# Kernel optimization log

Hardware: AMD Instinct MI355X
Metric: run time of the kernel (lower is better)

Reference implementation:

```python
import jax, jax.numpy as jnp
import numpy as np

LN_EPS = 1e-5   # torch nn.LayerNorm default
R_EPS = 1e-8    # eps used in log(R.clamp(min=eps))


def layernorm(x, g, b):
    mu = jnp.mean(x, axis=-1, keepdims=True)
    var = jnp.var(x, axis=-1, keepdims=True)
    return (x - mu) * jax.lax.rsqrt(var + LN_EPS) * g + b


def setup_inputs() -> dict:
    S, B, C, h, w, d = 4, 1, 128, 10, 10, 10
    nL = 2  # num_layers
    key = jax.random.key(0)
    ks = jax.random.split(key, 20)
    std = 0.02
    inp = {
        "z": jax.random.normal(ks[0], (S, B, C, h, w, d), jnp.float32),
        "r": jax.random.uniform(ks[1], (S,), jnp.float32, 0.1, 1.0),
        "seq_embed": std * jax.random.normal(ks[2], (S, C), jnp.float32),
        # per-layer attention params, stacked on leading layer axis
        "Wq": std * jax.random.normal(ks[3], (nL, C, C), jnp.float32),
        "Wk": std * jax.random.normal(ks[4], (nL, C, C), jnp.float32),
        "Wv": std * jax.random.normal(ks[5], (nL, C, C), jnp.float32),
        "Wp": std * jax.random.normal(ks[6], (nL, C, C), jnp.float32),
        "beta": jnp.ones((nL,), jnp.float32),
        "ln1_g": jnp.ones((nL, C), jnp.float32),
        "ln1_b": jnp.zeros((nL, C), jnp.float32),
        # FFN params
        "ffn_w1": std * jax.random.normal(ks[7], (C, 4 * C), jnp.float32),
        "ffn_b1": jnp.zeros((4 * C,), jnp.float32),
        "ffn_w2": std * jax.random.normal(ks[8], (4 * C, C), jnp.float32),
        "ffn_b2": jnp.zeros((C,), jnp.float32),
        "ln2_g": jnp.ones((C,), jnp.float32),
        "ln2_b": jnp.zeros((C,), jnp.float32),
    }
    return inp


def _forward(z, r, seq_embed, Wq, Wk, Wv, Wp, beta, ln1_g, ln1_b,
             ffn_w1, ffn_b1, ffn_w2, ffn_b2, ln2_g, ln2_b):
    S, B, C, h, w, d = z.shape
    N = h * w * d
    L = S * N
    nL, _, _ = Wq.shape
    H = 8
    Dh = C // H
    scale = Dh ** (-0.5)

    # tokenize: [S,B,C,h,w,d] -> [B, S*N, C] with per-sequence embedding added
    tokens = z.reshape(S, B, C, N).transpose(1, 0, 3, 2)      # [B,S,N,C]
    tokens = tokens + seq_embed[None, :, None, :]
    tokens = tokens.reshape(B, L, C)

    # reliability bias: log(clamp(outer(r_tok, r_tok), eps))  [L,L]
    r_tok = jnp.repeat(r, N)                                   # [L]
    log_R = jnp.log(jnp.clip(r_tok[:, None] * r_tok[None, :], R_EPS, None))

    for l in range(nL):
        residual = tokens
        Q = (tokens @ Wq[l]).reshape(B, L, H, Dh)
        K = (tokens @ Wk[l]).reshape(B, L, H, Dh)
        V = (tokens @ Wv[l]).reshape(B, L, H, Dh)
        attn = jnp.einsum('bihd,bjhd->bhij', Q, K) * scale     # [B,H,L,L]
        attn = attn + beta[l] * log_R[None, None]
        attn = jax.nn.softmax(attn, axis=-1)
        out = jnp.einsum('bhij,bjhd->bihd', attn, V).reshape(B, L, C)
        out = out @ Wp[l]
        tokens = layernorm(out + residual, ln1_g[l], ln1_b[l])

    # FFN (exact GELU, matching torch nn.GELU default) + residual + LN
    hdn = jax.nn.gelu(tokens @ ffn_w1 + ffn_b1, approximate=False)
    tokens = layernorm((hdn @ ffn_w2 + ffn_b2) + tokens, ln2_g, ln2_b)

    # de-tokenize: [B,L,C] -> [B, S*C, h, w, d]
    tokens = tokens.reshape(B, S, N, C).transpose(0, 1, 3, 2)  # [B,S,C,N]
    return tokens.reshape(B, S * C, h, w, d)


def reference(z, r, seq_embed, Wq, Wk, Wv, Wp, beta, ln1_g, ln1_b,
              ffn_w1, ffn_b1, ffn_w2, ffn_b2, ln2_g, ln2_b):
    return _forward(z, r, seq_embed, Wq, Wk, Wv, Wp, beta, ln1_g, ln1_b,
                    ffn_w1, ffn_b1, ffn_w2, ffn_b2, ln2_g, ln2_b)
```

## Files before the change

kernel.cpp:

```cpp
#include <hip/hip_runtime.h>
#include <hip/hip_bf16.h>
#include <math.h>

#define LL 4000
#define CC 128
#define NN 1000
#define NLAYER 2
#define KSPLIT 4
#define SCLOG2 0.36067376022224085f
#define KROW 20
#define VROW 36

typedef __attribute__((ext_vector_type(4))) short bf16x4;
typedef __attribute__((ext_vector_type(8))) short short8;
typedef __attribute__((ext_vector_type(4))) float f32x4;
typedef __attribute__((ext_vector_type(2))) unsigned int u32x2;

__device__ __forceinline__ short bf16rne(float f) {
    return __builtin_bit_cast(short, __float2bfloat16(f));
}
__device__ __forceinline__ float bf16tof(short s) {
    return __builtin_bit_cast(float, (unsigned)((unsigned short)s) << 16);
}

__device__ __forceinline__ bf16x4 pack4(const float* p) {
    unsigned w01 = __builtin_amdgcn_perm(__builtin_bit_cast(unsigned, p[1]),
                                         __builtin_bit_cast(unsigned, p[0]),
                                         0x07060302u);
    unsigned w23 = __builtin_amdgcn_perm(__builtin_bit_cast(unsigned, p[3]),
                                         __builtin_bit_cast(unsigned, p[2]),
                                         0x07060302u);
    u32x2 w = {w01, w23};
    return __builtin_bit_cast(bf16x4, w);
}

__global__ void prep_tok_kernel(const float* __restrict__ Wq, const float* __restrict__ Wk,
                                const float* __restrict__ Wv, const float* __restrict__ Wp,
                                const float* __restrict__ w1, const float* __restrict__ w2,
                                const float* __restrict__ r, const float* __restrict__ beta,
                                short* __restrict__ wt8, short* __restrict__ w1t,
                                short* __restrict__ w2t, float* __restrict__ kbw,
                                const float* __restrict__ z, const float* __restrict__ se,
                                float* __restrict__ tok, short* __restrict__ tokb) {
    __shared__ float tl[32][33];
    const int bid = blockIdx.x;
    if (bid < 1025) {
        int idx = bid * 256 + threadIdx.x;
        if (idx < 8 * 16384) {
            int m = idx >> 14, i = idx & 16383;
            int n = i >> 7, k = i & 127;
            const float* src = (m < 2) ? Wq + (size_t)m * 16384
                             : (m < 4) ? Wk + (size_t)(m - 2) * 16384
                             : (m < 6) ? Wv + (size_t)(m - 4) * 16384
                                       : Wp + (size_t)(m - 6) * 16384;
            wt8[idx] = bf16rne(src[k * 128 + n]);
        } else if (idx < 8 * 16384 + 65536) {
            int i = idx - 8 * 16384;
            int n = i >> 7, k = i & 127;
            w1t[i] = bf16rne(w1[(size_t)k * 512 + n]);
        } else if (idx < 8 * 16384 + 2 * 65536) {
            int i = idx - 8 * 16384 - 65536;
            int n = i >> 9, k = i & 511;
            w2t[i] = bf16rne(w2[(size_t)k * 128 + n]);
        } else if (idx < 8 * 16384 + 2 * 65536 + NLAYER * KSPLIT) {
            int i = idx - (8 * 16384 + 2 * 65536);
            int l = i / KSPLIT, zz = i - l * KSPLIT;
            kbw[i] = exp2f(beta[l] * __log2f(r[zz]));
        }
    } else {
        int b2 = bid - 1025;
        const int n0 = (b2 & 31) * 32;
        const int c0 = ((b2 >> 5) & 3) * 32;
        const int s  = b2 >> 7;
        const int tx = threadIdx.x & 31, ty = threadIdx.x >> 5;
        #pragma unroll
        for (int i = 0; i < 4; ++i) {
            int n = n0 + tx;
            if (n < NN) tl[ty * 4 + i][tx] = z[((size_t)s * CC + c0 + ty * 4 + i) * NN + n];
        }
        __syncthreads();
        #pragma unroll
        for (int i = 0; i < 4; ++i) {
            int n = n0 + ty * 4 + i;
            if (n < NN) {
                int c = c0 + tx;
                float v = tl[tx][ty * 4 + i] + se[s * CC + c];
                size_t o = ((size_t)(s * NN + n)) * CC + c;
                tok[o] = v;
                tokb[o] = bf16rne(v);
            }
        }
    }
}

__global__ void detok_kernel(const float* __restrict__ tok,
                             float* __restrict__ out) {
    __shared__ float tl[32][33];
    const int s  = blockIdx.z;
    const int c0 = blockIdx.y * 32;
    const int n0 = blockIdx.x * 32;
    const int tx = threadIdx.x & 31, ty = threadIdx.x >> 5;
    #pragma unroll
    for (int i = 0; i < 4; ++i) {
        int n = n0 + ty * 4 + i;
        if (n < NN) tl[ty * 4 + i][tx] = tok[((size_t)(s * NN + n)) * CC + c0 + tx];
    }
    __syncthreads();
    #pragma unroll
    for (int i = 0; i < 4; ++i) {
        int n = n0 + tx;
        if (n < NN) out[((size_t)s * CC + c0 + ty * 4 + i) * NN + n] = tl[tx][ty * 4 + i];
    }
}

__device__ __forceinline__ void gemm_body(
        const short* __restrict__ A, const short* __restrict__ Wt,
        const float* __restrict__ bias, void* __restrict__ outp,
        int M, int K, int N, int flags, int row0, int col0) {
    __shared__ short Al[16][136];
    __shared__ short Wl[128][136];
    const int tid = threadIdx.x;
    const int lane = tid & 63;
    const int w = tid >> 6;
    const int lq = lane & 15, g = lane >> 4;

    f32x4 acc[2] = {{0.f,0.f,0.f,0.f},{0.f,0.f,0.f,0.f}};

    for (int kc = 0; kc < K; kc += 128) {
        {
            int r = tid >> 4, c = (tid & 15) * 8;
            *(short8*)&Al[r][c] = *(const short8*)(A + (size_t)(row0 + r) * K + kc + c);
        }
        {
            int c = (tid & 15) * 8;
            int nb = tid >> 4;
            #pragma unroll
            for (int i = 0; i < 8; ++i) {
                int n = nb + i * 16;
                *(short8*)&Wl[n][c] = *(const short8*)(Wt + (size_t)(col0 + n) * K + kc + c);
            }
        }
        __syncthreads();
        bf16x4 af[8];
        #pragma unroll
        for (int ks = 0; ks < 8; ++ks)
            af[ks] = *(const bf16x4*)&Al[lq][ks * 16 + g * 4];
        #pragma unroll
        for (int ct = 0; ct < 2; ++ct) {
            int n = (w * 2 + ct) * 16 + lq;
            #pragma unroll
            for (int ks = 0; ks < 8; ++ks) {
                bf16x4 bfr = *(const bf16x4*)&Wl[n][ks * 16 + g * 4];
                acc[ct] = __builtin_amdgcn_mfma_f32_16x16x16bf16_1k(af[ks], bfr, acc[ct], 0, 0, 0);
            }
        }
        __syncthreads();
    }
    #pragma unroll
    for (int ct = 0; ct < 2; ++ct) {
        int col = col0 + (w * 2 + ct) * 16 + lq;
        float bv = bias ? bias[col] : 0.f;
        float v[4];
        #pragma unroll
        for (int r = 0; r < 4; ++r) {
            v[r] = acc[ct][r] + bv;
            if (flags & 2) v[r] = 0.5f * v[r] * (1.f + erff(v[r] * 0.70710678118654752f));
            if (flags & 8) v[r] *= SCLOG2;
        }
        if (flags & 4) {
            bf16x4 res = {bf16rne(v[0]), bf16rne(v[1]), bf16rne(v[2]), bf16rne(v[3])};
            *(bf16x4*)((short*)outp + (size_t)col * M + row0 + g * 4) = res;
        } else if (flags & 16) {
            #pragma unroll
            for (int r = 0; r < 4; ++r)
                ((short*)outp)[((size_t)(col >> 4) * M + (row0 + g * 4 + r)) * 16 + (col & 15)] = bf16rne(v[r]);
        } else if (flags & 1) {
            #pragma unroll
            for (int r = 0; r < 4; ++r)
                ((short*)outp)[(size_t)(row0 + g * 4 + r) * N + col] = bf16rne(v[r]);
        } else {
            #pragma unroll
            for (int r = 0; r < 4; ++r)
                ((float*)outp)[(size_t)(row0 + g * 4 + r) * N + col] = v[r];
        }
    }
}

__global__ __launch_bounds__(256) void mfma_gemm3(
        const short* __restrict__ A,
        const short* __restrict__ W0, const short* __restrict__ W1,
        const short* __restrict__ W2,
        short* __restrict__ o0, short* __restrict__ o1, short* __restrict__ o2,
        int M, int K, int N) {
    const short* Wt = (blockIdx.z == 0) ? W0 : (blockIdx.z == 1) ? W1 : W2;
    short* o = (blockIdx.z == 0) ? o0 : (blockIdx.z == 1) ? o1 : o2;
    int flags = (blockIdx.z == 0) ? (1 | 8) : (blockIdx.z == 1) ? 16 : 4;
    gemm_body(A, Wt, nullptr, o, M, K, N, flags, blockIdx.x * 16, 0);
}

__global__ __launch_bounds__(256) void mfma_gemm_ln_cmb(
        const short* __restrict__ pob, const float* __restrict__ pl,
        const short* __restrict__ Wt, const float* __restrict__ resid,
        const float* __restrict__ gam, const float* __restrict__ bet,
        float* __restrict__ outf, short* __restrict__ outb) {
    __shared__ short Al[16][136];
    __shared__ short Wl[128][136];
    __shared__ float sL[4][4][4], s2L[4][4][4];
    const int tid = threadIdx.x;
    const int lane = tid & 63;
    const int w = tid >> 6;
    const int lq = lane & 15, g = lane >> 4;
    const int row0 = blockIdx.x * 16;

    {
        int r = tid >> 4, c0 = (tid & 15) * 8;
        int row = row0 + r;
        int h = c0 >> 4;
        float a8[8] = {0.f,0.f,0.f,0.f,0.f,0.f,0.f,0.f};
        float den = 0.f;
        #pragma unroll
        for (int zz = 0; zz < KSPLIT; ++zz) {
            short8 t = *(const short8*)(pob + (size_t)zz * LL * CC + (size_t)row * CC + c0);
            #pragma unroll
            for (int j = 0; j < 8; ++j) a8[j] += bf16tof(t[j]);
            den += pl[(zz * 8 + h) * LL + row];
        }
        float inv = 1.f / den;
        short8 packed;
        #pragma unroll
        for (int j = 0; j < 8; ++j) packed[j] = bf16rne(a8[j] * inv);
        *(short8*)&Al[r][c0] = packed;
    }
    {
        int c = (tid & 15) * 8;
        int nb = tid >> 4;
        #pragma unroll
        for (int i = 0; i < 8; ++i) {
            int n = nb + i * 16;
            *(short8*)&Wl[n][c] = *(const short8*)(Wt + (size_t)n * CC + c);
        }
    }
    __syncthreads();

    f32x4 acc[2] = {{0.f,0.f,0.f,0.f},{0.f,0.f,0.f,0.f}};
    bf16x4 af[8];
    #pragma unroll
    for (int ks = 0; ks < 8; ++ks)
        af[ks] = *(const bf16x4*)&Al[lq][ks * 16 + g * 4];
    #pragma unroll
    for (int ct = 0; ct < 2; ++ct) {
        int n = (w * 2 + ct) * 16 + lq;
        #pragma unroll
        for (int ks = 0; ks < 8; ++ks) {
            bf16x4 bfr = *(const bf16x4*)&Wl[n][ks * 16 + g * 4];
            acc[ct] = __builtin_amdgcn_mfma_f32_16x16x16bf16_1k(af[ks], bfr, acc[ct], 0, 0, 0);
        }
    }

    float v[2][4];
    int cols[2] = {(w * 2) * 16 + lq, (w * 2 + 1) * 16 + lq};
    #pragma unroll
    for (int ct = 0; ct < 2; ++ct) {
        #pragma unroll
        for (int r = 0; r < 4; ++r)
            v[ct][r] = acc[ct][r] +
                       resid[(size_t)(row0 + g * 4 + r) * CC + cols[ct]];
    }
    float sr[4], s2r[4];
    #pragma unroll
    for (int r = 0; r < 4; ++r) {
        sr[r]  = v[0][r] + v[1][r];
        s2r[r] = v[0][r] * v[0][r] + v[1][r] * v[1][r];
    }
    #pragma unroll
    for (int off = 1; off < 16; off <<= 1) {
        #pragma unroll
        for (int r = 0; r < 4; ++r) {
            sr[r]  += __shfl_xor(sr[r],  off);
            s2r[r] += __shfl_xor(s2r[r], off);
        }
    }
    if (lq == 0) {
        #pragma unroll
        for (int r = 0; r < 4; ++r) { sL[w][g][r] = sr[r]; s2L[w][g][r] = s2r[r]; }
    }
    __syncthreads();
    #pragma unroll
    for (int r = 0; r < 4; ++r) {
        float s = 0.f, s2 = 0.f;
        #pragma unroll
        for (int ww = 0; ww < 4; ++ww) { s += sL[ww][g][r]; s2 += s2L[ww][g][r]; }
        float mu = s * (1.f / CC);
        float var = s2 * (1.f / CC) - mu * mu;
        float rstd = rsqrtf(var + 1e-5f);
        size_t rowoff = (size_t)(row0 + g * 4 + r) * CC;
        #pragma unroll
        for (int ct = 0; ct < 2; ++ct) {
            float y = (v[ct][r] - mu) * rstd * gam[cols[ct]] + bet[cols[ct]];
            outf[rowoff + cols[ct]] = y;
            outb[rowoff + cols[ct]] = bf16rne(y);
        }
    }
}

__global__ __launch_bounds__(256) void fused_ffn(
        const short* __restrict__ tokb, const short* __restrict__ w1t,
        const float* __restrict__ b1, const short* __restrict__ w2t,
        const float* __restrict__ b2, const float* __restrict__ resid,
        const float* __restrict__ gam, const float* __restrict__ bet,
        float* __restrict__ outf, short* __restrict__ outb) {
    __shared__ short Al[16][136];
    __shared__ short Wl[128][136];
    __shared__ short Hl[16][520];
    __shared__ float sL[4][4][4], s2L[4][4][4];
    const int tid = threadIdx.x;
    const int lane = tid & 63;
    const int w = tid >> 6;
    const int lq = lane & 15, g = lane >> 4;
    const int row0 = blockIdx.x * 16;

    {
        int r = tid >> 4, c = (tid & 15) * 8;
        *(short8*)&Al[r][c] = *(const short8*)(tokb + (size_t)(row0 + r) * CC + c);
    }

    bf16x4 af[8];
    for (int cc = 0; cc < 4; ++cc) {
        {
            int c = (tid & 15) * 8;
            int nb = tid >> 4;
            #pragma unroll
            for (int i = 0; i < 8; ++i) {
                int n = nb + i * 16;
                *(short8*)&Wl[n][c] = *(const short8*)(w1t + (size_t)(cc * 128 + n) * CC + c);
            }
        }
        __syncthreads();
        if (cc == 0) {
            #pragma unroll
            for (int ks = 0; ks < 8; ++ks)
                af[ks] = *(const bf16x4*)&Al[lq][ks * 16 + g * 4];
        }
        f32x4 acc[2] = {{0.f,0.f,0.f,0.f},{0.f,0.f,0.f,0.f}};
        #pragma unroll
        for (int ct = 0; ct < 2; ++ct) {
            int n = (w * 2 + ct) * 16 + lq;
            #pragma unroll
            for (int ks = 0; ks < 8; ++ks) {
                bf16x4 bfr = *(const bf16x4*)&Wl[n][ks * 16 + g * 4];
                acc[ct] = __builtin_amdgcn_mfma_f32_16x16x16bf16_1k(af[ks], bfr, acc[ct], 0, 0, 0);
            }
        }
        #pragma unroll
        for (int ct = 0; ct < 2; ++ct) {
            int col = (w * 2 + ct) * 16 + lq;
            float bv = b1[cc * 128 + col];
            #pragma unroll
            for (int r = 0; r < 4; ++r) {
                float v = acc[ct][r] + bv;
                v = 0.5f * v * (1.f + erff(v * 0.70710678118654752f));
                Hl[g * 4 + r][cc * 128 + col] = bf16rne(v);
            }
        }
        __syncthreads();
    }

    f32x4 acc2[2] = {{0.f,0.f,0.f,0.f},{0.f,0.f,0.f,0.f}};
    for (int kc = 0; kc < 4; ++kc) {
        {
            int c = (tid & 15) * 8;
            int nb = tid >> 4;
            #pragma unroll
            for (int i = 0; i < 8; ++i) {
                int n = nb + i * 16;
                *(short8*)&Wl[n][c] = *(const short8*)(w2t + (size_t)n * 512 + kc * 128 + c);
            }
        }
        __syncthreads();
        bf16x4 hf[8];
        #pragma unroll
        for (int ks = 0; ks < 8; ++ks)
            hf[ks] = *(const bf16x4*)&Hl[lq][kc * 128 + ks * 16 + g * 4];
        #pragma unroll
        for (int ct = 0; ct < 2; ++ct) {
            int n = (w * 2 + ct) * 16 + lq;
            #pragma unroll
            for (int ks = 0; ks < 8; ++ks) {
                bf16x4 bfr = *(const bf16x4*)&Wl[n][ks * 16 + g * 4];
                acc2[ct] = __builtin_amdgcn_mfma_f32_16x16x16bf16_1k(hf[ks], bfr, acc2[ct], 0, 0, 0);
            }
        }
        __syncthreads();
    }

    float v[2][4];
    int cols[2] = {(w * 2) * 16 + lq, (w * 2 + 1) * 16 + lq};
    #pragma unroll
    for (int ct = 0; ct < 2; ++ct) {
        float bv = b2[cols[ct]];
        #pragma unroll
        for (int r = 0; r < 4; ++r)
            v[ct][r] = acc2[ct][r] + bv +
                       resid[(size_t)(row0 + g * 4 + r) * CC + cols[ct]];
    }
    float sr[4], s2r[4];
    #pragma unroll
    for (int r = 0; r < 4; ++r) {
        sr[r]  = v[0][r] + v[1][r];
        s2r[r] = v[0][r] * v[0][r] + v[1][r] * v[1][r];
    }
    #pragma unroll
    for (int off = 1; off < 16; off <<= 1) {
        #pragma unroll
        for (int r = 0; r < 4; ++r) {
            sr[r]  += __shfl_xor(sr[r],  off);
            s2r[r] += __shfl_xor(s2r[r], off);
        }
    }
    if (lq == 0) {
        #pragma unroll
        for (int r = 0; r < 4; ++r) { sL[w][g][r] = sr[r]; s2L[w][g][r] = s2r[r]; }
    }
    __syncthreads();
    #pragma unroll
    for (int r = 0; r < 4; ++r) {
        float s = 0.f, s2 = 0.f;
        #pragma unroll
        for (int ww = 0; ww < 4; ++ww) { s += sL[ww][g][r]; s2 += s2L[ww][g][r]; }
        float mu = s * (1.f / CC);
        float var = s2 * (1.f / CC) - mu * mu;
        float rstd = rsqrtf(var + 1e-5f);
        size_t rowoff = (size_t)(row0 + g * 4 + r) * CC;
        #pragma unroll
        for (int ct = 0; ct < 2; ++ct) {
            float y = (v[ct][r] - mu) * rstd * gam[cols[ct]] + bet[cols[ct]];
            outf[rowoff + cols[ct]] = y;
            outb[rowoff + cols[ct]] = bf16rne(y);
        }
    }
}

__global__ __launch_bounds__(256) void attn_mfma_kernel(
        const short* __restrict__ Qb, const short* __restrict__ Kh,
        const short* __restrict__ Vt, const float* __restrict__ kbw,
        short* __restrict__ pob, float* __restrict__ pl) {
    __shared__ short Kl[2][32][KROW];
    __shared__ short Vl[2][16][VROW];
    const int tid  = threadIdx.x;
    const int lane = tid & 63;
    const int wv   = tid >> 6;
    const int lq = lane & 15;
    const int g  = lane >> 4;
    const int h  = blockIdx.y;
    const int z  = blockIdx.z;
    const int qtA = blockIdx.x * 8 + wv * 2;
    const int qtB = qtA + 1;
    const bool qvA = qtA < LL / 16;
    const bool qvB = qtB < LL / 16;
    const int hd0 = h * 16;
    const int kbase = z * NN;

    bf16x4 qfA = {0, 0, 0, 0}, qfB = {0, 0, 0, 0};
    if (qvA) qfA = *(const bf16x4*)(Qb + (size_t)(qtA * 16 + lq) * CC + hd0 + 4 * g);
    if (qvB) qfB = *(const bf16x4*)(Qb + (size_t)(qtB * 16 + lq) * CC + hd0 + 4 * g);

    const short onev = (lq == 0) ? (short)0x3F80 : (short)0;
    const bf16x4 af1 = {onev, onev, onev, onev};

    const short* kgp = Kh + ((size_t)h * LL + kbase) * 16 + tid * 2;
    const short* vgp = Vt + (size_t)(hd0 + (tid >> 4)) * LL + kbase + (tid & 15) * 2;
    short* kwp = &Kl[0][0][0] + (tid >> 3) * KROW + (tid & 7) * 2;
    short* vwp = &Vl[0][0][0] + (tid >> 4) * VROW + (tid & 15) * 2;
    const int kbufstride = 32 * KROW;
    const int vbufstride = 16 * VROW;

    f32x4 oA  = {0.f, 0.f, 0.f, 0.f}, oB  = {0.f, 0.f, 0.f, 0.f};
    f32x4 psA = {0.f, 0.f, 0.f, 0.f}, psB = {0.f, 0.f, 0.f, 0.f};

    {
        unsigned kd = *(const unsigned*)kgp;
        unsigned vd = *(const unsigned*)vgp;
        *(unsigned*)kwp = kd;
        *(unsigned*)vwp = vd;
    }
    unsigned kdA = *(const unsigned*)(kgp + (size_t)32 * 16);
    unsigned vdA = *(const unsigned*)(vgp + 32);
    __syncthreads();

    for (int t = 0; t < 31; ++t) {
        unsigned kdB, vdB;
        if (t < 30) {
            kdB = *(const unsigned*)(kgp + (size_t)(t + 2) * 32 * 16);
            vdB = *(const unsigned*)(vgp + (t + 2) * 32);
        }
        {
            const short* kb = &Kl[t & 1][0][0];
            const short* vb = &Vl[t & 1][0][0];
            bf16x4 K0 = *(const bf16x4*)(kb + lq * KROW + 4 * g);
            bf16x4 K1 = *(const bf16x4*)(kb + (16 + lq) * KROW + 4 * g);
            bf16x4 V0 = *(const bf16x4*)(vb + lq * VROW + 4 * g);
            bf16x4 V1 = *(const bf16x4*)(vb + lq * VROW + 16 + 4 * g);
            const f32x4 zz = {0.f, 0.f, 0.f, 0.f};
            f32x4 sA0 = __builtin_amdgcn_mfma_f32_16x16x16bf16_1k(K0, qfA, zz, 0, 0, 0);
            f32x4 sA1 = __builtin_amdgcn_mfma_f32_16x16x16bf16_1k(K1, qfA, zz, 0, 0, 0);
            f32x4 sB0 = __builtin_amdgcn_mfma_f32_16x16x16bf16_1k(K0, qfB, zz, 0, 0, 0);
            f32x4 sB1 = __builtin_amdgcn_mfma_f32_16x16x16bf16_1k(K1, qfB, zz, 0, 0, 0);
            float pA0[4], pA1[4], pB0[4], pB1[4];
            #pragma unroll
            for (int r = 0; r < 4; ++r) {
                pA0[r] = __builtin_amdgcn_exp2f(sA0[r]);
                pA1[r] = __builtin_amdgcn_exp2f(sA1[r]);
                pB0[r] = __builtin_amdgcn_exp2f(sB0[r]);
                pB1[r] = __builtin_amdgcn_exp2f(sB1[r]);
            }
            bf16x4 ptA0 = pack4(pA0), ptA1 = pack4(pA1);
            bf16x4 ptB0 = pack4(pB0), ptB1 = pack4(pB1);
            oA  = __builtin_amdgcn_mfma_f32_16x16x16bf16_1k(V0, ptA0, oA, 0, 0, 0);
            oA  = __builtin_amdgcn_mfma_f32_16x16x16bf16_1k(V1, ptA1, oA, 0, 0, 0);
            oB  = __builtin_amdgcn_mfma_f32_16x16x16bf16_1k(V0, ptB0, oB, 0, 0, 0);
            oB  = __builtin_amdgcn_mfma_f32_16x16x16bf16_1k(V1, ptB1, oB, 0, 0, 0);
            psA = __builtin_amdgcn_mfma_f32_16x16x16bf16_1k(af1, ptA0, psA, 0, 0, 0);
            psA = __builtin_amdgcn_mfma_f32_16x16x16bf16_1k(af1, ptA1, psA, 0, 0, 0);
            psB = __builtin_amdgcn_mfma_f32_16x16x16bf16_1k(af1, ptB0, psB, 0, 0, 0);
            psB = __builtin_amdgcn_mfma_f32_16x16x16bf16_1k(af1, ptB1, psB, 0, 0, 0);
        }
        const int nb = (t + 1) & 1;
        *(unsigned*)(kwp + nb * kbufstride) = kdA;
        *(unsigned*)(vwp + nb * vbufstride) = vdA;
        __syncthreads();
        if (t < 30) { kdA = kdB; vdA = vdB; }
    }

    {
        const short* kb = &Kl[1][0][0];
        const short* vb = &Vl[1][0][0];
        bf16x4 K0 = *(const bf16x4*)(kb + lq * KROW + 4 * g);
        bf16x4 V0 = *(const bf16x4*)(vb + lq * VROW + 4 * g);
        if (g >= 2) V0 = (bf16x4){0, 0, 0, 0};
        const f32x4 zz = {0.f, 0.f, 0.f, 0.f};
        f32x4 sA0 = __builtin_amdgcn_mfma_f32_16x16x16bf16_1k(K0, qfA, zz, 0, 0, 0);
        f32x4 sB0 = __builtin_amdgcn_mfma_f32_16x16x16bf16_1k(K0, qfB, zz, 0, 0, 0);
        float pA0[4], pB0[4];
        #pragma unroll
        for (int r = 0; r < 4; ++r) {
            pA0[r] = (g < 2) ? __builtin_amdgcn_exp2f(sA0[r]) : 0.f;
            pB0[r] = (g < 2) ? __builtin_amdgcn_exp2f(sB0[r]) : 0.f;
        }
        bf16x4 ptA0 = pack4(pA0), ptB0 = pack4(pB0);
        oA  = __builtin_amdgcn_mfma_f32_16x16x16bf16_1k(V0, ptA0, oA, 0, 0, 0);
        oB  = __builtin_amdgcn_mfma_f32_16x16x16bf16_1k(V0, ptB0, oB, 0, 0, 0);
        psA = __builtin_amdgcn_mfma_f32_16x16x16bf16_1k(af1, ptA0, psA, 0, 0, 0);
        psB = __builtin_amdgcn_mfma_f32_16x16x16bf16_1k(af1, ptB0, psB, 0, 0, 0);
    }

    const float wz = kbw[z];
    if (qvA) {
        bf16x4 ow = {bf16rne(oA[0] * wz), bf16rne(oA[1] * wz),
                     bf16rne(oA[2] * wz), bf16rne(oA[3] * wz)};
        *(bf16x4*)(pob + (size_t)z * LL * CC + (size_t)(qtA * 16 + lq) * CC + hd0 + 4 * g) = ow;
        if (g == 0) pl[(z * 8 + h) * LL + qtA * 16 + lq] = psA[0] * wz;
    }
    if (qvB) {
        bf16x4 ow = {bf16rne(oB[0] * wz), bf16rne(oB[1] * wz),
                     bf16rne(oB[2] * wz), bf16rne(oB[3] * wz)};
        *(bf16x4*)(pob + (size_t)z * LL * CC + (size_t)(qtB * 16 + lq) * CC + hd0 + 4 * g) = ow;
        if (g == 0) pl[(z * 8 + h) * LL + qtB * 16 + lq] = psB[0] * wz;
    }
}

extern "C" void kernel_launch(void* const* d_in, const int* in_sizes, int n_in,
                              void* d_out, int out_size, void* d_ws, size_t ws_size,
                              hipStream_t stream) {
    const float* z    = (const float*)d_in[0];
    const float* r    = (const float*)d_in[1];
    const float* se   = (const float*)d_in[2];
    const float* Wq   = (const float*)d_in[3];
    const float* Wk   = (const float*)d_in[4];
    const float* Wv   = (const float*)d_in[5];
    const float* Wp   = (const float*)d_in[6];
    const float* beta = (const float*)d_in[7];
    const float* ln1g = (const float*)d_in[8];
    const float* ln1b = (const float*)d_in[9];
    const float* w1   = (const float*)d_in[10];
    const float* b1   = (const float*)d_in[11];
    const float* w2   = (const float*)d_in[12];
    const float* b2   = (const float*)d_in[13];
    const float* ln2g = (const float*)d_in[14];
    const float* ln2b = (const float*)d_in[15];
    float* out = (float*)d_out;

    float* ws   = (float*)d_ws;
    float* tok  = ws;
    float* kbw  = tok + LL * CC;
    float* pl   = kbw + 8;
    short* pob  = (short*)(pl + KSPLIT * 8 * LL);
    short* tokb = pob + (size_t)KSPLIT * LL * CC;
    short* Qb   = tokb + LL * CC;
    short* Kh   = Qb   + LL * CC;
    short* Vt   = Kh   + LL * CC + 1024;
    short* wt8  = Vt   + LL * CC + 1024;
    short* w1t  = wt8  + 8 * 16384;
    short* w2t  = w1t  + 65536;

    prep_tok_kernel<<<1537, 256, 0, stream>>>(Wq, Wk, Wv, Wp, w1, w2, r, beta,
                                              wt8, w1t, w2t, kbw, z, se, tok, tokb);

    for (int l = 0; l < NLAYER; ++l) {
        const short* wqt = wt8 + (size_t)(0 * 2 + l) * 16384;
        const short* wkt = wt8 + (size_t)(1 * 2 + l) * 16384;
        const short* wvt = wt8 + (size_t)(2 * 2 + l) * 16384;
        const short* wpt = wt8 + (size_t)(3 * 2 + l) * 16384;
        mfma_gemm3<<<dim3(LL / 16, 1, 3), 256, 0, stream>>>(
            tokb, wqt, wkt, wvt, Qb, Kh, Vt, LL, CC, CC);
        attn_mfma_kernel<<<dim3((LL / 16 + 7) / 8, 8, KSPLIT), 256, 0, stream>>>(
            Qb, Kh, Vt, kbw + l * KSPLIT, pob, pl);
        mfma_gemm_ln_cmb<<<LL / 16, 256, 0, stream>>>(
            pob, pl, wpt, tok, ln1g + l * CC, ln1b + l * CC, tok, tokb);
    }

    fused_ffn<<<LL / 16, 256, 0, stream>>>(
        tokb, w1t, b1, w2t, b2, tok, ln2g, ln2b, tok, tokb);

    detok_kernel<<<dim3(32, 4, 4), 256, 0, stream>>>(tok, out);
}
```

Baseline: 94.61 us.

## Fuse attention combine+proj+LN with next-layer QKV and with FFN

Unrolls the two-layer loop. The layer-0 output projection, LayerNorm and combine are fused with the layer-1 Q/K/V projections, and the layer-1 projection+LN is fused with the FFN and final LN. This removes two kernel launches and the global round-trips of the bf16 token buffer and the reloaded residual. In exchange each fused block does more serial work with extra barriers and loses some parallelism across grid.z.

```diff
diff --git a/kernel.cpp b/kernel.cpp
--- a/kernel.cpp
+++ b/kernel.cpp
@@ -198,11 +198,97 @@
     gemm_body(A, Wt, nullptr, o, M, K, N, flags, blockIdx.x * 16, 0);
 }
 
-__global__ __launch_bounds__(256) void mfma_gemm_ln_cmb(
+__device__ __forceinline__ void combine_stage(
         const short* __restrict__ pob, const float* __restrict__ pl,
-        const short* __restrict__ Wt, const float* __restrict__ resid,
+        short (*Al)[136], int row0, int tid) {
+    int r = tid >> 4, c0 = (tid & 15) * 8;
+    int row = row0 + r;
+    int h = c0 >> 4;
+    float a8[8] = {0.f,0.f,0.f,0.f,0.f,0.f,0.f,0.f};
+    float den = 0.f;
+    #pragma unroll
+    for (int zz = 0; zz < KSPLIT; ++zz) {
+        short8 t = *(const short8*)(pob + (size_t)zz * LL * CC + (size_t)row * CC + c0);
+        #pragma unroll
+        for (int j = 0; j < 8; ++j) a8[j] += bf16tof(t[j]);
+        den += pl[(zz * 8 + h) * LL + row];
+    }
+    float inv = 1.f / den;
+    short8 packed;
+    #pragma unroll
+    for (int j = 0; j < 8; ++j) packed[j] = bf16rne(a8[j] * inv);
+    *(short8*)&Al[r][c0] = packed;
+}
+
+__device__ __forceinline__ void w_stage(const short* __restrict__ Wt, int ldw,
+                                        int koff, short (*Wl)[136], int tid) {
+    int c = (tid & 15) * 8;
+    int nb = tid >> 4;
+    #pragma unroll
+    for (int i = 0; i < 8; ++i) {
+        int n = nb + i * 16;
+        *(short8*)&Wl[n][c] = *(const short8*)(Wt + (size_t)n * ldw + koff + c);
+    }
+}
+
+__device__ __forceinline__ void tile_mfma(const bf16x4 af[8], short (*Wl)[136],
+                                          f32x4 acc[2], int w, int lq, int g) {
+    #pragma unroll
+    for (int ct = 0; ct < 2; ++ct) {
+        int n = (w * 2 + ct) * 16 + lq;
+        #pragma unroll
+        for (int ks = 0; ks < 8; ++ks) {
+            bf16x4 bfr = *(const bf16x4*)&Wl[n][ks * 16 + g * 4];
+            acc[ct] = __builtin_amdgcn_mfma_f32_16x16x16bf16_1k(af[ks], bfr, acc[ct], 0, 0, 0);
+        }
+    }
+}
+
+__device__ __forceinline__ void ln_compute(
+        float v[2][4], float y[2][4], const float* __restrict__ gam,
+        const float* __restrict__ bet, float (*sL)[4][4], float (*s2L)[4][4],
+        int w, int lq, int g, const int cols[2]) {
+    float sr[4], s2r[4];
+    #pragma unroll
+    for (int r = 0; r < 4; ++r) {
+        sr[r]  = v[0][r] + v[1][r];
+        s2r[r] = v[0][r] * v[0][r] + v[1][r] * v[1][r];
+    }
+    #pragma unroll
+    for (int off = 1; off < 16; off <<= 1) {
+        #pragma unroll
+        for (int r = 0; r < 4; ++r) {
+            sr[r]  += __shfl_xor(sr[r],  off);
+            s2r[r] += __shfl_xor(s2r[r], off);
+        }
+    }
+    if (lq == 0) {
+        #pragma unroll
+        for (int r = 0; r < 4; ++r) { sL[w][g][r] = sr[r]; s2L[w][g][r] = s2r[r]; }
+    }
+    __syncthreads();
+    #pragma unroll
+    for (int r = 0; r < 4; ++r) {
+        float s = 0.f, s2 = 0.f;
+        #pragma unroll
+        for (int ww = 0; ww < 4; ++ww) { s += sL[ww][g][r]; s2 += s2L[ww][g][r]; }
+        float mu = s * (1.f / CC);
+        float var = s2 * (1.f / CC) - mu * mu;
+        float rstd = rsqrtf(var + 1e-5f);
+        #pragma unroll
+        for (int ct = 0; ct < 2; ++ct)
+            y[ct][r] = (v[ct][r] - mu) * rstd * gam[cols[ct]] + bet[cols[ct]];
+    }
+}
+
+__global__ __launch_bounds__(256) void mfma_cmb_ln_qkv(
+        const short* __restrict__ pob, const float* __restrict__ pl,
+        const short* __restrict__ Wpt, const float* __restrict__ resid,
         const float* __restrict__ gam, const float* __restrict__ bet,
-        float* __restrict__ outf, short* __restrict__ outb) {
+        float* __restrict__ outf,
+        const short* __restrict__ Wqt, const short* __restrict__ Wkt,
+        const short* __restrict__ Wvt,
+        short* __restrict__ Qb, short* __restrict__ Kh, short* __restrict__ Vt) {
     __shared__ short Al[16][136];
     __shared__ short Wl[128][136];
     __shared__ float sL[4][4][4], s2L[4][4][4];
@@ -212,103 +298,87 @@
     const int lq = lane & 15, g = lane >> 4;
     const int row0 = blockIdx.x * 16;
 
-    {
-        int r = tid >> 4, c0 = (tid & 15) * 8;
-        int row = row0 + r;
-        int h = c0 >> 4;
-        float a8[8] = {0.f,0.f,0.f,0.f,0.f,0.f,0.f,0.f};
-        float den = 0.f;
-        #pragma unroll
-        for (int zz = 0; zz < KSPLIT; ++zz) {
-            short8 t = *(const short8*)(pob + (size_t)zz * LL * CC + (size_t)row * CC + c0);
-            #pragma unroll
-            for (int j = 0; j < 8; ++j) a8[j] += bf16tof(t[j]);
-            den += pl[(zz * 8 + h) * LL + row];
-        }
-        float inv = 1.f / den;
-        short8 packed;
-        #pragma unroll
-        for (int j = 0; j < 8; ++j) packed[j] = bf16rne(a8[j] * inv);
-        *(short8*)&Al[r][c0] = packed;
-    }
-    {
-        int c = (tid & 15) * 8;
-        int nb = tid >> 4;
-        #pragma unroll
-        for (int i = 0; i < 8; ++i) {
-            int n = nb + i * 16;
-            *(short8*)&Wl[n][c] = *(const short8*)(Wt + (size_t)n * CC + c);
-        }
-    }
-    __syncthreads();
-
-    f32x4 acc[2] = {{0.f,0.f,0.f,0.f},{0.f,0.f,0.f,0.f}};
+    combine_stage(pob, pl, Al, row0, tid);
+    w_stage(Wpt, CC, 0, Wl, tid);
+    __syncthreads();
+
     bf16x4 af[8];
     #pragma unroll
     for (int ks = 0; ks < 8; ++ks)
         af[ks] = *(const bf16x4*)&Al[lq][ks * 16 + g * 4];
-    #pragma unroll
-    for (int ct = 0; ct < 2; ++ct) {
-        int n = (w * 2 + ct) * 16 + lq;
-        #pragma unroll
-        for (int ks = 0; ks < 8; ++ks) {
-            bf16x4 bfr = *(const bf16x4*)&Wl[n][ks * 16 + g * 4];
-            acc[ct] = __builtin_amdgcn_mfma_f32_16x16x16bf16_1k(af[ks], bfr, acc[ct], 0, 0, 0);
-        }
-    }
-
-    float v[2][4];
+    f32x4 acc[2] = {{0.f,0.f,0.f,0.f},{0.f,0.f,0.f,0.f}};
+    tile_mfma(af, Wl, acc, w, lq, g);
+
+    float v[2][4], y[2][4];
     int cols[2] = {(w * 2) * 16 + lq, (w * 2 + 1) * 16 + lq};
     #pragma unroll
-    for (int ct = 0; ct < 2; ++ct) {
+    for (int ct = 0; ct < 2; ++ct)
         #pragma unroll
         for (int r = 0; r < 4; ++r)
-            v[ct][r] = acc[ct][r] +
-                       resid[(size_t)(row0 + g * 4 + r) * CC + cols[ct]];
-    }
-    float sr[4], s2r[4];
-    #pragma unroll
-    for (int r = 0; r < 4; ++r) {
-        sr[r]  = v[0][r] + v[1][r];
-        s2r[r] = v[0][r] * v[0][r] + v[1][r] * v[1][r];
-    }
-    #pragma unroll
-    for (int off = 1; off < 16; off <<= 1) {
+            v[ct][r] = acc[ct][r] + resid[(size_t)(row0 + g * 4 + r) * CC + cols[ct]];
+    ln_compute(v, y, gam, bet, sL, s2L, w, lq, g, cols);
+
+    #pragma unroll
+    for (int ct = 0; ct < 2; ++ct)
         #pragma unroll
         for (int r = 0; r < 4; ++r) {
-            sr[r]  += __shfl_xor(sr[r],  off);
-            s2r[r] += __shfl_xor(s2r[r], off);
-        }
-    }
-    if (lq == 0) {
-        #pragma unroll
-        for (int r = 0; r < 4; ++r) { sL[w][g][r] = sr[r]; s2L[w][g][r] = s2r[r]; }
-    }
-    __syncthreads();
-    #pragma unroll
-    for (int r = 0; r < 4; ++r) {
-        float s = 0.f, s2 = 0.f;
-        #pragma unroll
-        for (int ww = 0; ww < 4; ++ww) { s += sL[ww][g][r]; s2 += s2L[ww][g][r]; }
-        float mu = s * (1.f / CC);
-        float var = s2 * (1.f / CC) - mu * mu;
-        float rstd = rsqrtf(var + 1e-5f);
-        size_t rowoff = (size_t)(row0 + g * 4 + r) * CC;
+            outf[(size_t)(row0 + g * 4 + r) * CC + cols[ct]] = y[ct][r];
+            Al[g * 4 + r][cols[ct]] = bf16rne(y[ct][r]);
+        }
+    __syncthreads();
+
+    bf16x4 af2[8];
+    #pragma unroll
+    for (int ks = 0; ks < 8; ++ks)
+        af2[ks] = *(const bf16x4*)&Al[lq][ks * 16 + g * 4];
+
+    __syncthreads();
+    w_stage(Wqt, CC, 0, Wl, tid);
+    __syncthreads();
+    {
+        f32x4 aq[2] = {{0.f,0.f,0.f,0.f},{0.f,0.f,0.f,0.f}};
+        tile_mfma(af2, Wl, aq, w, lq, g);
+        #pragma unroll
+        for (int ct = 0; ct < 2; ++ct)
+            #pragma unroll
+            for (int r = 0; r < 4; ++r)
+                Qb[(size_t)(row0 + g * 4 + r) * CC + cols[ct]] = bf16rne(aq[ct][r] * SCLOG2);
+    }
+    __syncthreads();
+    w_stage(Wkt, CC, 0, Wl, tid);
+    __syncthreads();
+    {
+        f32x4 ak[2] = {{0.f,0.f,0.f,0.f},{0.f,0.f,0.f,0.f}};
+        tile_mfma(af2, Wl, ak, w, lq, g);
+        #pragma unroll
+        for (int ct = 0; ct < 2; ++ct)
+            #pragma unroll
+            for (int r = 0; r < 4; ++r)
+                Kh[((size_t)(cols[ct] >> 4) * LL + (row0 + g * 4 + r)) * 16 + (cols[ct] & 15)] = bf16rne(ak[ct][r]);
+    }
+    __syncthreads();
+    w_stage(Wvt, CC, 0, Wl, tid);
+    __syncthreads();
+    {
+        f32x4 av[2] = {{0.f,0.f,0.f,0.f},{0.f,0.f,0.f,0.f}};
+        tile_mfma(af2, Wl, av, w, lq, g);
         #pragma unroll
         for (int ct = 0; ct < 2; ++ct) {
-            float y = (v[ct][r] - mu) * rstd * gam[cols[ct]] + bet[cols[ct]];
-            outf[rowoff + cols[ct]] = y;
-            outb[rowoff + cols[ct]] = bf16rne(y);
-        }
-    }
-}
-
-__global__ __launch_bounds__(256) void fused_ffn(
-        const short* __restrict__ tokb, const short* __restrict__ w1t,
-        const float* __restrict__ b1, const short* __restrict__ w2t,
-        const float* __restrict__ b2, const float* __restrict__ resid,
-        const float* __restrict__ gam, const float* __restrict__ bet,
-        float* __restrict__ outf, short* __restrict__ outb) {
+            bf16x4 res = {bf16rne(av[ct][0]), bf16rne(av[ct][1]),
+                          bf16rne(av[ct][2]), bf16rne(av[ct][3])};
+            *(bf16x4*)(Vt + (size_t)cols[ct] * LL + row0 + g * 4) = res;
+        }
+    }
+}
+
+__global__ __launch_bounds__(256) void mfma_cmb_ln_ffn(
+        const short* __restrict__ pob, const float* __restrict__ pl,
+        const short* __restrict__ Wpt, const float* __restrict__ resid,
+        const float* __restrict__ g1, const float* __restrict__ be1,
+        const short* __restrict__ w1t, const float* __restrict__ b1,
+        const short* __restrict__ w2t, const float* __restrict__ b2,
+        const float* __restrict__ g2, const float* __restrict__ be2,
+        float* __restrict__ outf) {
     __shared__ short Al[16][136];
     __shared__ short Wl[128][136];
     __shared__ short Hl[16][520];
@@ -319,125 +389,84 @@
     const int lq = lane & 15, g = lane >> 4;
     const int row0 = blockIdx.x * 16;
 
-    {
-        int r = tid >> 4, c = (tid & 15) * 8;
-        *(short8*)&Al[r][c] = *(const short8*)(tokb + (size_t)(row0 + r) * CC + c);
-    }
+    combine_stage(pob, pl, Al, row0, tid);
+    w_stage(Wpt, CC, 0, Wl, tid);
+    __syncthreads();
 
     bf16x4 af[8];
+    #pragma unroll
+    for (int ks = 0; ks < 8; ++ks)
+        af[ks] = *(const bf16x4*)&Al[lq][ks * 16 + g * 4];
+    f32x4 acc[2] = {{0.f,0.f,0.f,0.f},{0.f,0.f,0.f,0.f}};
+    tile_mfma(af, Wl, acc, w, lq, g);
+
+    float v[2][4], y[2][4];
+    int cols[2] = {(w * 2) * 16 + lq, (w * 2 + 1) * 16 + lq};
+    #pragma unroll
+    for (int ct = 0; ct < 2; ++ct)
+        #pragma unroll
+        for (int r = 0; r < 4; ++r)
+            v[ct][r] = acc[ct][r] + resid[(size_t)(row0 + g * 4 + r) * CC + cols[ct]];
+    ln_compute(v, y, g1, be1, sL, s2L, w, lq, g, cols);
+
+    #pragma unroll
+    for (int ct = 0; ct < 2; ++ct)
+        #pragma unroll
+        for (int r = 0; r < 4; ++r)
+            Al[g * 4 + r][cols[ct]] = bf16rne(y[ct][r]);
+    __syncthreads();
+
+    bf16x4 af2[8];
+    #pragma unroll
+    for (int ks = 0; ks < 8; ++ks)
+        af2[ks] = *(const bf16x4*)&Al[lq][ks * 16 + g * 4];
+
     for (int cc = 0; cc < 4; ++cc) {
-        {
-            int c = (tid & 15) * 8;
-            int nb = tid >> 4;
-            #pragma unroll
-            for (int i = 0; i < 8; ++i) {
-                int n = nb + i * 16;
-                *(short8*)&Wl[n][c] = *(const short8*)(w1t + (size_t)(cc * 128 + n) * CC + c);
-            }
-        }
-        __syncthreads();
-        if (cc == 0) {
-            #pragma unroll
-            for (int ks = 0; ks < 8; ++ks)
-                af[ks] = *(const bf16x4*)&Al[lq][ks * 16 + g * 4];
-        }
-        f32x4 acc[2] = {{0.f,0.f,0.f,0.f},{0.f,0.f,0.f,0.f}};
-        #pragma unroll
-        for (int ct = 0; ct < 2; ++ct) {
-            int n = (w * 2 + ct) * 16 + lq;
-            #pragma unroll
-            for (int ks = 0; ks < 8; ++ks) {
-                bf16x4 bfr = *(const bf16x4*)&Wl[n][ks * 16 + g * 4];
-                acc[ct] = __builtin_amdgcn_mfma_f32_16x16x16bf16_1k(af[ks], bfr, acc[ct], 0, 0, 0);
-            }
-        }
+        __syncthreads();
+        w_stage(w1t + (size_t)cc * 128 * CC, CC, 0, Wl, tid);
+        __syncthreads();
+        f32x4 a1[2] = {{0.f,0.f,0.f,0.f},{0.f,0.f,0.f,0.f}};
+        tile_mfma(af2, Wl, a1, w, lq, g);
         #pragma unroll
         for (int ct = 0; ct < 2; ++ct) {
             int col = (w * 2 + ct) * 16 + lq;
             float bv = b1[cc * 128 + col];
             #pragma unroll
             for (int r = 0; r < 4; ++r) {
-                float v = acc[ct][r] + bv;
-                v = 0.5f * v * (1.f + erff(v * 0.70710678118654752f));
-                Hl[g * 4 + r][cc * 128 + col] = bf16rne(v);
+                float vv = a1[ct][r] + bv;
+                vv = 0.5f * vv * (1.f + erff(vv * 0.70710678118654752f));
+                Hl[g * 4 + r][cc * 128 + col] = bf16rne(vv);
             }
         }
-        __syncthreads();
-    }
+    }
+    __syncthreads();
 
     f32x4 acc2[2] = {{0.f,0.f,0.f,0.f},{0.f,0.f,0.f,0.f}};
     for (int kc = 0; kc < 4; ++kc) {
-        {
-            int c = (tid & 15) * 8;
-            int nb = tid >> 4;
-            #pragma unroll
-            for (int i = 0; i < 8; ++i) {
-                int n = nb + i * 16;
-                *(short8*)&Wl[n][c] = *(const short8*)(w2t + (size_t)n * 512 + kc * 128 + c);
-            }
-        }
+        w_stage(w2t, 512, kc * 128, Wl, tid);
         __syncthreads();
         bf16x4 hf[8];
         #pragma unroll
         for (int ks = 0; ks < 8; ++ks)
             hf[ks] = *(const bf16x4*)&Hl[lq][kc * 128 + ks * 16 + g * 4];
-        #pragma unroll
-        for (int ct = 0; ct < 2; ++ct) {
-            int n = (w * 2 + ct) * 16 + lq;
-            #pragma unroll
-            for (int ks = 0; ks < 8; ++ks) {
-                bf16x4 bfr = *(const bf16x4*)&Wl[n][ks * 16 + g * 4];
-                acc2[ct] = __builtin_amdgcn_mfma_f32_16x16x16bf16_1k(hf[ks], bfr, acc2[ct], 0, 0, 0);
-            }
-        }
-        __syncthreads();
-    }
-
-    float v[2][4];
-    int cols[2] = {(w * 2) * 16 + lq, (w * 2 + 1) * 16 + lq};
+        tile_mfma(hf, Wl, acc2, w, lq, g);
+        __syncthreads();
+    }
+
+    float v2[2][4], y2[2][4];
     #pragma unroll
     for (int ct = 0; ct < 2; ++ct) {
         float bv = b2[cols[ct]];
         #pragma unroll
         for (int r = 0; r < 4; ++r)
-            v[ct][r] = acc2[ct][r] + bv +
-                       resid[(size_t)(row0 + g * 4 + r) * CC + cols[ct]];
-    }
-    float sr[4], s2r[4];
-    #pragma unroll
-    for (int r = 0; r < 4; ++r) {
-        sr[r]  = v[0][r] + v[1][r];
-        s2r[r] = v[0][r] * v[0][r] + v[1][r] * v[1][r];
-    }
-    #pragma unroll
-    for (int off = 1; off < 16; off <<= 1) {
-        #pragma unroll
-        for (int r = 0; r < 4; ++r) {
-            sr[r]  += __shfl_xor(sr[r],  off);
-            s2r[r] += __shfl_xor(s2r[r], off);
-        }
-    }
-    if (lq == 0) {
-        #pragma unroll
-        for (int r = 0; r < 4; ++r) { sL[w][g][r] = sr[r]; s2L[w][g][r] = s2r[r]; }
-    }
-    __syncthreads();
-    #pragma unroll
-    for (int r = 0; r < 4; ++r) {
-        float s = 0.f, s2 = 0.f;
-        #pragma unroll
-        for (int ww = 0; ww < 4; ++ww) { s += sL[ww][g][r]; s2 += s2L[ww][g][r]; }
-        float mu = s * (1.f / CC);
-        float var = s2 * (1.f / CC) - mu * mu;
-        float rstd = rsqrtf(var + 1e-5f);
-        size_t rowoff = (size_t)(row0 + g * 4 + r) * CC;
-        #pragma unroll
-        for (int ct = 0; ct < 2; ++ct) {
-            float y = (v[ct][r] - mu) * rstd * gam[cols[ct]] + bet[cols[ct]];
-            outf[rowoff + cols[ct]] = y;
-            outb[rowoff + cols[ct]] = bf16rne(y);
-        }
-    }
+            v2[ct][r] = acc2[ct][r] + bv + y[ct][r];
+    }
+    ln_compute(v2, y2, g2, be2, sL, s2L, w, lq, g, cols);
+    #pragma unroll
+    for (int ct = 0; ct < 2; ++ct)
+        #pragma unroll
+        for (int r = 0; r < 4; ++r)
+            outf[(size_t)(row0 + g * 4 + r) * CC + cols[ct]] = y2[ct][r];
 }
 
 __global__ __launch_bounds__(256) void attn_mfma_kernel(
@@ -602,24 +631,30 @@
     short* w1t  = wt8  + 8 * 16384;
     short* w2t  = w1t  + 65536;
 
+    const short* wq0 = wt8 + (size_t)0 * 16384;
+    const short* wq1 = wt8 + (size_t)1 * 16384;
+    const short* wk0 = wt8 + (size_t)2 * 16384;
+    const short* wk1 = wt8 + (size_t)3 * 16384;
+    const short* wv0 = wt8 + (size_t)4 * 16384;
+    const short* wv1 = wt8 + (size_t)5 * 16384;
+    const short* wp0 = wt8 + (size_t)6 * 16384;
+    const short* wp1 = wt8 + (size_t)7 * 16384;
+
     prep_tok_kernel<<<1537, 256, 0, stream>>>(Wq, Wk, Wv, Wp, w1, w2, r, beta,
                                               wt8, w1t, w2t, kbw, z, se, tok, tokb);
 
-    for (int l = 0; l < NLAYER; ++l) {
-        const short* wqt = wt8 + (size_t)(0 * 2 + l) * 16384;
-        const short* wkt = wt8 + (size_t)(1 * 2 + l) * 16384;
-        const short* wvt = wt8 + (size_t)(2 * 2 + l) * 16384;
-        const short* wpt = wt8 + (size_t)(3 * 2 + l) * 16384;
-        mfma_gemm3<<<dim3(LL / 16, 1, 3), 256, 0, stream>>>(
-            tokb, wqt, wkt, wvt, Qb, Kh, Vt, LL, CC, CC);
-        attn_mfma_kernel<<<dim3((LL / 16 + 7) / 8, 8, KSPLIT), 256, 0, stream>>>(
-            Qb, Kh, Vt, kbw + l * KSPLIT, pob, pl);
-        mfma_gemm_ln_cmb<<<LL / 16, 256, 0, stream>>>(
-            pob, pl, wpt, tok, ln1g + l * CC, ln1b + l * CC, tok, tokb);
-    }
-
-    fused_ffn<<<LL / 16, 256, 0, stream>>>(
-        tokb, w1t, b1, w2t, b2, tok, ln2g, ln2b, tok, tokb);
+    mfma_gemm3<<<dim3(LL / 16, 1, 3), 256, 0, stream>>>(
+        tokb, wq0, wk0, wv0, Qb, Kh, Vt, LL, CC, CC);
+    attn_mfma_kernel<<<dim3((LL / 16 + 7) / 8, 8, KSPLIT), 256, 0, stream>>>(
+        Qb, Kh, Vt, kbw + 0 * KSPLIT, pob, pl);
+    mfma_cmb_ln_qkv<<<LL / 16, 256, 0, stream>>>(
+        pob, pl, wp0, tok, ln1g + 0 * CC, ln1b + 0 * CC, tok,
+        wq1, wk1, wv1, Qb, Kh, Vt);
+    attn_mfma_kernel<<<dim3((LL / 16 + 7) / 8, 8, KSPLIT), 256, 0, stream>>>(
+        Qb, Kh, Vt, kbw + 1 * KSPLIT, pob, pl);
+    mfma_cmb_ln_ffn<<<LL / 16, 256, 0, stream>>>(
+        pob, pl, wp1, tok, ln1g + 1 * CC, ln1b + 1 * CC,
+        w1t, b1, w2t, b2, ln2g, ln2b, tok);
 
     detok_kernel<<<dim3(32, 4, 4), 256, 0, stream>>>(tok, out);
 }
```

Result: faster. 90.42 us (-4.4%).
